# Performance work log

Measured on AMD Instinct MI355X. Metric: run time of the kernel, lower is better.

The kernel has to match this reference:

```python
import jax, jax.numpy as jnp
import numpy as np

B, L, S, DE, D = 16, 2048, 1024, 512, 256
VOP, NSIL, A, NN = 64, 8, 64, 100000


def setup_inputs() -> dict:
    key = jax.random.key(0)
    ks = jax.random.split(key, 11)
    return {
        "encoded_sentence_tokens": jax.random.normal(ks[0], (B, S, DE), jnp.float32),
        "encoded_stack_nodes": jax.random.normal(ks[1], (NN, D), jnp.float32),
        "silent_embeddings": jax.random.normal(ks[2], (NSIL, D), jnp.float32),
        "op_embedding": jax.random.normal(ks[3], (VOP, D), jnp.float32) * 0.02,
        "w_shift": jax.random.normal(ks[4], (DE, D), jnp.float32) / np.sqrt(DE).astype(np.float32),
        "b_shift": jnp.zeros((D,), jnp.float32),
        "op_tokens": jax.random.randint(ks[5], (B, L), 0, VOP),
        "arg_idx": jax.random.randint(ks[6], (B, L), 0, NSIL + A),
        "shift_idx": jax.random.randint(ks[7], (B, L), 0, S),
        "item_type": jax.random.randint(ks[8], (B, L), 0, 3),
        "avail_nodes": jax.random.randint(ks[9], (B, L, A), 0, NN),
    }


def reference(encoded_sentence_tokens, encoded_stack_nodes, silent_embeddings,
              op_embedding, w_shift, b_shift,
              op_tokens, arg_idx, shift_idx, item_type, avail_nodes):
    # Operation embeddings: [B, L, D]
    emb_ops = op_embedding[op_tokens]

    # Shift-arg embeddings: gather sentence encodings per (b, l), then linear. [B, L, D]
    gathered_sent = jnp.take_along_axis(
        encoded_sentence_tokens, shift_idx[:, :, None], axis=1)  # [B, L, DE]
    emb_shift = jnp.einsum('ble,ed->bld', gathered_sent, w_shift) + b_shift

    # Argument embeddings: choice index < NSIL -> silent embedding, else stack node.
    # Equivalent to concat([silent, available_node_embs], axis=2)[arg_idx] without
    # materializing the [B, L, NSIL+A, D] choice tensor.
    is_silent = arg_idx < NSIL                                    # [B, L]
    silent_sel = silent_embeddings[jnp.clip(arg_idx, 0, NSIL - 1)]  # [B, L, D]
    node_pos = jnp.clip(arg_idx - NSIL, 0, A - 1)                 # [B, L]
    node_ids = jnp.take_along_axis(avail_nodes, node_pos[:, :, None], axis=2)[..., 0]
    node_sel = encoded_stack_nodes[node_ids]                      # [B, L, D]
    emb_args = jnp.where(is_silent[:, :, None], silent_sel, node_sel)

    # combine_embeddings: positional masks align, so it's a 3-way select by type.
    t = item_type[:, :, None]
    result = jnp.where(t == 0, emb_ops,
             jnp.where(t == 1, emb_args,
             jnp.where(t == 2, emb_shift, jnp.zeros_like(emb_ops))))
    return result
```

## Files before the change

### kernel.cpp

```cpp
#include <hip/hip_runtime.h>

#define B_    16
#define L_    2048
#define S_    1024
#define DE_   512
#define D_    256
#define NSIL_ 8
#define A_    64
#define MS_   (B_ * S_)

#define BM 128
#define BN 64
#define BK 64

typedef __attribute__((ext_vector_type(8))) short  short8;
typedef __attribute__((ext_vector_type(4))) float  f32x4;

__device__ __forceinline__ unsigned short f2bf(float f) {
    unsigned int x = __builtin_bit_cast(unsigned int, f);
    x += 0x7fffu + ((x >> 16) & 1u);
    return (unsigned short)(x >> 16);
}

__global__ __launch_bounds__(256) void srse_wt(
    const float* __restrict__ w, unsigned short* __restrict__ wT)
{
    const int k = blockIdx.x;
    const int n = threadIdx.x;
    wT[n * DE_ + k] = f2bf(w[k * D_ + n]);
}

__global__ __launch_bounds__(256) void srse_gemm(
    const float*          __restrict__ sent,
    const unsigned short* __restrict__ wT,
    const float*          __restrict__ bsh,
    float*                __restrict__ P)
{
    __shared__ alignas(16) unsigned short As[BM * BK];
    __shared__ alignas(16) unsigned short Bs[BN * BK];

    const int nwg  = (MS_ / BM) * (D_ / BN);
    const int wg   = (blockIdx.x & 7) * (nwg / 8) + (blockIdx.x >> 3);
    const int bm   = wg >> 2;
    const int bn   = wg & 3;
    const int gm0  = bm * BM;
    const int gn0  = bn * BN;

    const int t    = threadIdx.x;
    const int lane = t & 63;
    const int wid  = t >> 6;
    const int wm   = wid & 1;
    const int wn   = wid >> 1;
    const int fr   = lane & 15;
    const int fq   = lane >> 4;

    f32x4 acc[4][2] = {};

    for (int k0 = 0; k0 < DE_; k0 += BK) {
        #pragma unroll
        for (int s = 0; s < 4; ++s) {
            const int id  = s * 256 + t;
            const int row = id >> 3;
            const int k8  = id & 7;
            const float4 a0 = *(const float4*)(sent + (size_t)(gm0 + row) * DE_ + k0 + k8 * 8);
            const float4 a1 = *(const float4*)(sent + (size_t)(gm0 + row) * DE_ + k0 + k8 * 8 + 4);
            short8 v;
            v[0] = f2bf(a0.x); v[1] = f2bf(a0.y); v[2] = f2bf(a0.z); v[3] = f2bf(a0.w);
            v[4] = f2bf(a1.x); v[5] = f2bf(a1.y); v[6] = f2bf(a1.z); v[7] = f2bf(a1.w);
            const int widx = (row * BK + k8 * 8) ^ ((row & 7) << 3);
            *(short8*)(As + widx) = v;
        }
        #pragma unroll
        for (int s = 0; s < 2; ++s) {
            const int id = s * 256 + t;
            const int n  = id >> 3;
            const int k8 = id & 7;
            short8 v = *(const short8*)(wT + (size_t)(gn0 + n) * DE_ + k0 + k8 * 8);
            const int widx = (n * BK + k8 * 8) ^ ((n & 7) << 3);
            *(short8*)(Bs + widx) = v;
        }
        __syncthreads();

        #pragma unroll
        for (int ks = 0; ks < 2; ++ks) {
            short8 af[4], bf[2];
            #pragma unroll
            for (int mf = 0; mf < 4; ++mf) {
                const int row = wm * 64 + mf * 16 + fr;
                af[mf] = *(const short8*)(As + ((row * BK + ks * 32 + fq * 8) ^ ((row & 7) << 3)));
            }
            #pragma unroll
            for (int nf = 0; nf < 2; ++nf) {
                const int n = wn * 32 + nf * 16 + fr;
                bf[nf] = *(const short8*)(Bs + ((n * BK + ks * 32 + fq * 8) ^ ((n & 7) << 3)));
            }
            #pragma unroll
            for (int mf = 0; mf < 4; ++mf)
                #pragma unroll
                for (int nf = 0; nf < 2; ++nf)
                    acc[mf][nf] = __builtin_amdgcn_mfma_f32_16x16x32_bf16(
                        af[mf], bf[nf], acc[mf][nf], 0, 0, 0);
        }
        __syncthreads();
    }

    #pragma unroll
    for (int nf = 0; nf < 2; ++nf) {
        const int col = gn0 + wn * 32 + nf * 16 + fr;
        const float bval = bsh[col];
        #pragma unroll
        for (int mf = 0; mf < 4; ++mf) {
            #pragma unroll
            for (int r = 0; r < 4; ++r) {
                const int row = gm0 + wm * 64 + mf * 16 + fq * 4 + r;
                P[(size_t)row * D_ + col] = acc[mf][nf][r] + bval;
            }
        }
    }
}

__global__ __launch_bounds__(256) void srse_select(
    const float* __restrict__ P,
    const float* __restrict__ op_emb,
    const float* __restrict__ silent,
    const float* __restrict__ nodes,
    const int*   __restrict__ op_tokens,
    const int*   __restrict__ arg_idx,
    const int*   __restrict__ shift_idx,
    const int*   __restrict__ item_type,
    const int*   __restrict__ avail,
    float*       __restrict__ out)
{
    const int wid  = threadIdx.x >> 6;
    const int lane = threadIdx.x & 63;
    const int r0   = blockIdx.x * 32 + wid * 8;

    const float* src[8];
    #pragma unroll
    for (int i = 0; i < 8; ++i) {
        const int row = r0 + i;
        const int tt  = item_type[row];
        const int a   = arg_idx[row];
        int np = a - NSIL_;
        np = np < 0 ? 0 : (np > A_ - 1 ? A_ - 1 : np);
        const float* s0 = op_emb + (size_t)op_tokens[row] * D_;
        const float* s1 = (a < NSIL_)
                          ? silent + (size_t)a * D_
                          : nodes + (size_t)avail[(size_t)row * A_ + np] * D_;
        const float* s2 = P + (size_t)((row >> 11) * S_ + shift_idx[row]) * D_;
        src[i] = (tt == 0) ? s0 : ((tt == 1) ? s1 : s2);
    }

    float4 v[8];
    #pragma unroll
    for (int i = 0; i < 8; ++i)
        v[i] = *(const float4*)(src[i] + lane * 4);

    #pragma unroll
    for (int i = 0; i < 8; ++i)
        *(float4*)(out + (size_t)(r0 + i) * D_ + lane * 4) = v[i];
}

extern "C" void kernel_launch(void* const* d_in, const int* in_sizes, int n_in,
                              void* d_out, int out_size, void* d_ws, size_t ws_size,
                              hipStream_t stream) {
    const float* sent      = (const float*)d_in[0];
    const float* nodes     = (const float*)d_in[1];
    const float* silent    = (const float*)d_in[2];
    const float* op_emb    = (const float*)d_in[3];
    const float* w         = (const float*)d_in[4];
    const float* bsh       = (const float*)d_in[5];
    const int*   op_tokens = (const int*)d_in[6];
    const int*   arg_idx   = (const int*)d_in[7];
    const int*   shift_idx = (const int*)d_in[8];
    const int*   item_type = (const int*)d_in[9];
    const int*   avail     = (const int*)d_in[10];
    float*       out       = (float*)d_out;

    unsigned short* wT = (unsigned short*)d_ws;
    float*          P  = (float*)((char*)d_ws + D_ * DE_ * sizeof(unsigned short));

    srse_wt<<<DE_, 256, 0, stream>>>(w, wT);

    srse_gemm<<<(MS_ / BM) * (D_ / BN), 256, 0, stream>>>(sent, wT, bsh, P);

    srse_select<<<(B_ * L_) / 32, 256, 0, stream>>>(
        P, op_emb, silent, nodes, op_tokens, arg_idx, shift_idx, item_type,
        avail, out);
}
```

Before: 205.7 us.

## Fuse op/arg gathers into GEMM launch and store projection as bf16

```diff
diff --git a/kernel.cpp b/kernel.cpp
--- a/kernel.cpp
+++ b/kernel.cpp
@@ -12,6 +12,8 @@
 #define BM 128
 #define BN 64
 #define BK 64
+#define NGEMM 512
+#define NT01  256
 
 typedef __attribute__((ext_vector_type(8))) short  short8;
 typedef __attribute__((ext_vector_type(4))) float  f32x4;
@@ -20,6 +22,10 @@
     unsigned int x = __builtin_bit_cast(unsigned int, f);
     x += 0x7fffu + ((x >> 16) & 1u);
     return (unsigned short)(x >> 16);
+}
+__device__ __forceinline__ float bf2f(unsigned short u) {
+    unsigned int x = ((unsigned int)u) << 16;
+    return __builtin_bit_cast(float, x);
 }
 
 __global__ __launch_bounds__(256) void srse_wt(
@@ -30,135 +36,168 @@
     wT[n * DE_ + k] = f2bf(w[k * D_ + n]);
 }
 
-__global__ __launch_bounds__(256) void srse_gemm(
+__global__ __launch_bounds__(256) void srse_gemm_t01(
     const float*          __restrict__ sent,
     const unsigned short* __restrict__ wT,
     const float*          __restrict__ bsh,
-    float*                __restrict__ P)
+    unsigned short*       __restrict__ Pb,
+    const float*          __restrict__ op_emb,
+    const float*          __restrict__ silent,
+    const float*          __restrict__ nodes,
+    const int*            __restrict__ op_tokens,
+    const int*            __restrict__ arg_idx,
+    const int*            __restrict__ item_type,
+    const int*            __restrict__ avail,
+    float*                __restrict__ out)
 {
     __shared__ alignas(16) unsigned short As[BM * BK];
     __shared__ alignas(16) unsigned short Bs[BN * BK];
 
-    const int nwg  = (MS_ / BM) * (D_ / BN);
-    const int wg   = (blockIdx.x & 7) * (nwg / 8) + (blockIdx.x >> 3);
-    const int bm   = wg >> 2;
-    const int bn   = wg & 3;
-    const int gm0  = bm * BM;
-    const int gn0  = bn * BN;
-
     const int t    = threadIdx.x;
     const int lane = t & 63;
     const int wid  = t >> 6;
-    const int wm   = wid & 1;
-    const int wn   = wid >> 1;
-    const int fr   = lane & 15;
-    const int fq   = lane >> 4;
-
-    f32x4 acc[4][2] = {};
-
-    for (int k0 = 0; k0 < DE_; k0 += BK) {
+
+    if (blockIdx.x < NGEMM) {
+        const int wg  = (blockIdx.x & 7) * (NGEMM / 8) + (blockIdx.x >> 3);
+        const int bm  = wg >> 2;
+        const int bn  = wg & 3;
+        const int gm0 = bm * BM;
+        const int gn0 = bn * BN;
+
+        const int wm = wid & 1;
+        const int wn = wid >> 1;
+        const int fr = lane & 15;
+        const int fq = lane >> 4;
+
+        f32x4 acc[4][2] = {};
+
+        for (int k0 = 0; k0 < DE_; k0 += BK) {
+            #pragma unroll
+            for (int s = 0; s < 4; ++s) {
+                const int id  = s * 256 + t;
+                const int row = id >> 3;
+                const int k8  = id & 7;
+                const float4 a0 = *(const float4*)(sent + (size_t)(gm0 + row) * DE_ + k0 + k8 * 8);
+                const float4 a1 = *(const float4*)(sent + (size_t)(gm0 + row) * DE_ + k0 + k8 * 8 + 4);
+                short8 v;
+                v[0] = f2bf(a0.x); v[1] = f2bf(a0.y); v[2] = f2bf(a0.z); v[3] = f2bf(a0.w);
+                v[4] = f2bf(a1.x); v[5] = f2bf(a1.y); v[6] = f2bf(a1.z); v[7] = f2bf(a1.w);
+                const int widx = (row * BK + k8 * 8) ^ ((row & 7) << 3);
+                *(short8*)(As + widx) = v;
+            }
+            #pragma unroll
+            for (int s = 0; s < 2; ++s) {
+                const int id = s * 256 + t;
+                const int n  = id >> 3;
+                const int k8 = id & 7;
+                short8 v = *(const short8*)(wT + (size_t)(gn0 + n) * DE_ + k0 + k8 * 8);
+                const int widx = (n * BK + k8 * 8) ^ ((n & 7) << 3);
+                *(short8*)(Bs + widx) = v;
+            }
+            __syncthreads();
+
+            #pragma unroll
+            for (int ks = 0; ks < 2; ++ks) {
+                short8 af[4], bfr[2];
+                #pragma unroll
+                for (int mf = 0; mf < 4; ++mf) {
+                    const int row = wm * 64 + mf * 16 + fr;
+                    af[mf] = *(const short8*)(As + ((row * BK + ks * 32 + fq * 8) ^ ((row & 7) << 3)));
+                }
+                #pragma unroll
+                for (int nf = 0; nf < 2; ++nf) {
+                    const int n = wn * 32 + nf * 16 + fr;
+                    bfr[nf] = *(const short8*)(Bs + ((n * BK + ks * 32 + fq * 8) ^ ((n & 7) << 3)));
+                }
+                #pragma unroll
+                for (int mf = 0; mf < 4; ++mf)
+                    #pragma unroll
+                    for (int nf = 0; nf < 2; ++nf)
+                        acc[mf][nf] = __builtin_amdgcn_mfma_f32_16x16x32_bf16(
+                            af[mf], bfr[nf], acc[mf][nf], 0, 0, 0);
+            }
+            __syncthreads();
+        }
+
         #pragma unroll
-        for (int s = 0; s < 4; ++s) {
-            const int id  = s * 256 + t;
-            const int row = id >> 3;
-            const int k8  = id & 7;
-            const float4 a0 = *(const float4*)(sent + (size_t)(gm0 + row) * DE_ + k0 + k8 * 8);
-            const float4 a1 = *(const float4*)(sent + (size_t)(gm0 + row) * DE_ + k0 + k8 * 8 + 4);
-            short8 v;
-            v[0] = f2bf(a0.x); v[1] = f2bf(a0.y); v[2] = f2bf(a0.z); v[3] = f2bf(a0.w);
-            v[4] = f2bf(a1.x); v[5] = f2bf(a1.y); v[6] = f2bf(a1.z); v[7] = f2bf(a1.w);
-            const int widx = (row * BK + k8 * 8) ^ ((row & 7) << 3);
-            *(short8*)(As + widx) = v;
-        }
+        for (int nf = 0; nf < 2; ++nf) {
+            const int col = gn0 + wn * 32 + nf * 16 + fr;
+            const float bval = bsh[col];
+            #pragma unroll
+            for (int mf = 0; mf < 4; ++mf) {
+                #pragma unroll
+                for (int r = 0; r < 4; ++r) {
+                    const int row = gm0 + wm * 64 + mf * 16 + fq * 4 + r;
+                    Pb[(size_t)row * D_ + col] = f2bf(acc[mf][nf][r] + bval);
+                }
+            }
+        }
+    } else {
+        const int bid2 = blockIdx.x - NGEMM;
+        const int r0w  = bid2 * 128 + wid * 32;
+
         #pragma unroll
-        for (int s = 0; s < 2; ++s) {
-            const int id = s * 256 + t;
-            const int n  = id >> 3;
-            const int k8 = id & 7;
-            short8 v = *(const short8*)(wT + (size_t)(gn0 + n) * DE_ + k0 + k8 * 8);
-            const int widx = (n * BK + k8 * 8) ^ ((n & 7) << 3);
-            *(short8*)(Bs + widx) = v;
-        }
-        __syncthreads();
-
-        #pragma unroll
-        for (int ks = 0; ks < 2; ++ks) {
-            short8 af[4], bf[2];
-            #pragma unroll
-            for (int mf = 0; mf < 4; ++mf) {
-                const int row = wm * 64 + mf * 16 + fr;
-                af[mf] = *(const short8*)(As + ((row * BK + ks * 32 + fq * 8) ^ ((row & 7) << 3)));
-            }
-            #pragma unroll
-            for (int nf = 0; nf < 2; ++nf) {
-                const int n = wn * 32 + nf * 16 + fr;
-                bf[nf] = *(const short8*)(Bs + ((n * BK + ks * 32 + fq * 8) ^ ((n & 7) << 3)));
-            }
-            #pragma unroll
-            for (int mf = 0; mf < 4; ++mf)
-                #pragma unroll
-                for (int nf = 0; nf < 2; ++nf)
-                    acc[mf][nf] = __builtin_amdgcn_mfma_f32_16x16x32_bf16(
-                        af[mf], bf[nf], acc[mf][nf], 0, 0, 0);
-        }
-        __syncthreads();
+        for (int b4 = 0; b4 < 4; ++b4) {
+            const int r0 = r0w + b4 * 8;
+            const float* src[8];
+            int tt8[8];
+            #pragma unroll
+            for (int i = 0; i < 8; ++i) {
+                const int row = r0 + i;
+                const int tt  = item_type[row];
+                tt8[i] = tt;
+                const int a = arg_idx[row];
+                int np = a - NSIL_;
+                np = np < 0 ? 0 : (np > A_ - 1 ? A_ - 1 : np);
+                const float* s0 = op_emb + (size_t)op_tokens[row] * D_;
+                const float* s1 = (a < NSIL_)
+                                  ? silent + (size_t)a * D_
+                                  : nodes + (size_t)avail[(size_t)row * A_ + np] * D_;
+                src[i] = (tt == 0) ? s0 : s1;
+            }
+            float4 v[8];
+            #pragma unroll
+            for (int i = 0; i < 8; ++i)
+                v[i] = *(const float4*)(src[i] + lane * 4);
+            #pragma unroll
+            for (int i = 0; i < 8; ++i)
+                if (tt8[i] != 2)
+                    *(float4*)(out + (size_t)(r0 + i) * D_ + lane * 4) = v[i];
+        }
     }
-
-    #pragma unroll
-    for (int nf = 0; nf < 2; ++nf) {
-        const int col = gn0 + wn * 32 + nf * 16 + fr;
-        const float bval = bsh[col];
-        #pragma unroll
-        for (int mf = 0; mf < 4; ++mf) {
-            #pragma unroll
-            for (int r = 0; r < 4; ++r) {
-                const int row = gm0 + wm * 64 + mf * 16 + fq * 4 + r;
-                P[(size_t)row * D_ + col] = acc[mf][nf][r] + bval;
-            }
-        }
-    }
-}
-
-__global__ __launch_bounds__(256) void srse_select(
-    const float* __restrict__ P,
-    const float* __restrict__ op_emb,
-    const float* __restrict__ silent,
-    const float* __restrict__ nodes,
-    const int*   __restrict__ op_tokens,
-    const int*   __restrict__ arg_idx,
-    const int*   __restrict__ shift_idx,
-    const int*   __restrict__ item_type,
-    const int*   __restrict__ avail,
-    float*       __restrict__ out)
+}
+
+__global__ __launch_bounds__(256) void srse_t2(
+    const unsigned short* __restrict__ Pb,
+    const int*            __restrict__ shift_idx,
+    const int*            __restrict__ item_type,
+    float*                __restrict__ out)
 {
     const int wid  = threadIdx.x >> 6;
     const int lane = threadIdx.x & 63;
-    const int r0   = blockIdx.x * 32 + wid * 8;
-
-    const float* src[8];
+    const int r0   = blockIdx.x * 64 + wid * 16;
+
+    int tt[16], ss[16];
     #pragma unroll
-    for (int i = 0; i < 8; ++i) {
-        const int row = r0 + i;
-        const int tt  = item_type[row];
-        const int a   = arg_idx[row];
-        int np = a - NSIL_;
-        np = np < 0 ? 0 : (np > A_ - 1 ? A_ - 1 : np);
-        const float* s0 = op_emb + (size_t)op_tokens[row] * D_;
-        const float* s1 = (a < NSIL_)
-                          ? silent + (size_t)a * D_
-                          : nodes + (size_t)avail[(size_t)row * A_ + np] * D_;
-        const float* s2 = P + (size_t)((row >> 11) * S_ + shift_idx[row]) * D_;
-        src[i] = (tt == 0) ? s0 : ((tt == 1) ? s1 : s2);
+    for (int i = 0; i < 16; ++i) tt[i] = item_type[r0 + i];
+    #pragma unroll
+    for (int i = 0; i < 16; ++i) ss[i] = shift_idx[r0 + i];
+
+    #pragma unroll
+    for (int i = 0; i < 16; ++i) {
+        if (tt[i] == 2) {
+            const int row = r0 + i;
+            const int b   = row >> 11;
+            const unsigned short* p = Pb + (size_t)((b << 10) + ss[i]) * D_;
+            const short4 x = *(const short4*)(p + lane * 4);
+            float4 o;
+            o.x = bf2f((unsigned short)x.x);
+            o.y = bf2f((unsigned short)x.y);
+            o.z = bf2f((unsigned short)x.z);
+            o.w = bf2f((unsigned short)x.w);
+            *(float4*)(out + (size_t)row * D_ + lane * 4) = o;
+        }
     }
-
-    float4 v[8];
-    #pragma unroll
-    for (int i = 0; i < 8; ++i)
-        v[i] = *(const float4*)(src[i] + lane * 4);
-
-    #pragma unroll
-    for (int i = 0; i < 8; ++i)
-        *(float4*)(out + (size_t)(r0 + i) * D_ + lane * 4) = v[i];
 }
 
 extern "C" void kernel_launch(void* const* d_in, const int* in_sizes, int n_in,
@@ -178,13 +217,13 @@
     float*       out       = (float*)d_out;
 
     unsigned short* wT = (unsigned short*)d_ws;
-    float*          P  = (float*)((char*)d_ws + D_ * DE_ * sizeof(unsigned short));
+    unsigned short* Pb = (unsigned short*)((char*)d_ws + D_ * DE_ * 2);
 
     srse_wt<<<DE_, 256, 0, stream>>>(w, wT);
 
-    srse_gemm<<<(MS_ / BM) * (D_ / BN), 256, 0, stream>>>(sent, wT, bsh, P);
-
-    srse_select<<<(B_ * L_) / 32, 256, 0, stream>>>(
-        P, op_emb, silent, nodes, op_tokens, arg_idx, shift_idx, item_type,
-        avail, out);
-}
+    srse_gemm_t01<<<NGEMM + NT01, 256, 0, stream>>>(
+        sent, wT, bsh, Pb, op_emb, silent, nodes,
+        op_tokens, arg_idx, item_type, avail, out);
+
+    srse_t2<<<(B_ * L_) / 64, 256, 0, stream>>>(Pb, shift_idx, item_type, out);
+}
```

New measurement: 217.8 us. 1.06x slower.
